# Kernel tuning notes

Hardware: AMD Instinct MI355X
Metric: run time of the kernel (lower is better)

Reference implementation:

```python
import jax, jax.numpy as jnp
import numpy as np

TAU = 1.1      # LIF membrane time constant
ALPHA = 4.0    # sigmoid surrogate sharpness (spikingjelly default)
EPS = 1e-5     # BatchNorm eps
SCALE = 0.125  # attention scale


def lif(x, v_th):
    # Single-step LIF, v init 0, decay_input=True: v = x / tau; spike = H(v - v_th)
    # Straight-through: forward heaviside, backward sigmoid surrogate derivative.
    u = x / TAU - v_th
    sg = jax.nn.sigmoid(ALPHA * u)
    return sg + jax.lax.stop_gradient((u >= 0.0).astype(x.dtype) - sg)


def bn(x, gamma, beta):
    # BatchNorm1d in training mode on [B, C, N]: stats over (B, N) per channel
    mean = jnp.mean(x, axis=(0, 2), keepdims=True)
    var = jnp.var(x, axis=(0, 2), keepdims=True)
    return gamma[None, :, None] * (x - mean) * jax.lax.rsqrt(var + EPS) + beta[None, :, None]


def conv1x1(w, x):
    # Conv1d kernel_size=1: pointwise channel mix, x: [B,C,N], w: [O,C]
    return jnp.einsum('oc,bcn->bon', w, x)


def setup_inputs() -> dict:
    key = jax.random.key(0)
    B, C, N = 32, 512, 1024
    ks = jax.random.split(key, 6)
    s = 1.0 / np.sqrt(C)
    inp = {"x": jax.random.normal(ks[0], (B, C, N), jnp.float32)}
    for name, k in zip(["q", "k", "v", "proj"], ks[1:5]):
        inp[name + "_w"] = jax.random.uniform(k, (C, C), jnp.float32, -s, s)
        inp[name + "_gamma"] = jnp.ones((C,), jnp.float32)
        inp[name + "_beta"] = jnp.zeros((C,), jnp.float32)
    inp["proj_b"] = jax.random.uniform(ks[5], (C,), jnp.float32, -s, s)
    return inp


def reference(x, q_w, q_gamma, q_beta, k_w, k_gamma, k_beta, v_w, v_gamma, v_beta,
              proj_w, proj_b, proj_gamma, proj_beta):
    # x: [B, C, N]
    q = lif(bn(conv1x1(q_w, x), q_gamma, q_beta), 1.0)  # [B,C,N] spikes
    k = lif(bn(conv1x1(k_w, x), k_gamma, k_beta), 1.0)
    v = lif(bn(conv1x1(v_w, x), v_gamma, v_beta), 1.0)
    # linear (softmax-free) attention: kv[c,d] = sum_n k[n,c] v[n,d]
    kv = jnp.einsum('bcn,bdn->bcd', k, v)               # [B,C,C]
    attn = jnp.einsum('bcn,bcd->bdn', q, kv) * SCALE    # [B,C,N] (already transposed back)
    attn = lif(attn, 0.5)
    out = conv1x1(proj_w, attn) + proj_b[None, :, None]
    return lif(bn(out, proj_gamma, proj_beta), 1.0)
```

## Files before the change

kernel.cpp:

```cpp
#include <hip/hip_runtime.h>
#include <cstddef>


#define CC 512
#define BB 32
#define NN 1024

typedef __attribute__((ext_vector_type(4))) float v4f;
typedef __attribute__((ext_vector_type(2))) float v2f;
typedef __attribute__((ext_vector_type(4))) int v4i;
typedef __attribute__((ext_vector_type(8))) int v8i;
typedef unsigned char uchar;
typedef unsigned long long ull;

__device__ __forceinline__ uchar f2e4s(float v) {
  const uchar s = (v < 0.f) ? 0x80 : 0x00;
  float a = fabsf(v);
  if (a >= 464.f) return s | 0x7E;
  if (a < 0.015625f) {
    int q = (int)rintf(a * 512.f);
    return s | (uchar)q;
  }
  const int e = (int)((__float_as_uint(a) >> 23) & 0xFF) - 126;
  const float scale = __uint_as_float((unsigned)(4 - e + 127) << 23);
  const int q = (int)rintf(a * scale);
  int code = ((e - 1 + 7) << 3) + (q - 8);
  if (code > 0x7E) code = 0x7E;
  return s | (uchar)code;
}
__device__ __forceinline__ float e42f(uchar b) {
  const int e = (b >> 3) & 15, m = b & 7;
  const float mag = e ? __uint_as_float((unsigned)((e + 120) << 23) | ((unsigned)m << 20))
                      : (float)m * 0.001953125f;
  return (b & 0x80) ? -mag : mag;
}

__device__ __forceinline__ unsigned pk4_fp8(float a0, float a1, float a2, float a3) {
#if __has_builtin(__builtin_amdgcn_cvt_pk_fp8_f32)
  int r = __builtin_amdgcn_cvt_pk_fp8_f32(a0, a1, 0, false);
  r = __builtin_amdgcn_cvt_pk_fp8_f32(a2, a3, r, true);
  return (unsigned)r;
#else
  return (unsigned)f2e4s(a0) | ((unsigned)f2e4s(a1) << 8) |
         ((unsigned)f2e4s(a2) << 16) | ((unsigned)f2e4s(a3) << 24);
#endif
}
__device__ __forceinline__ uchar enc1(float v) {
#if __has_builtin(__builtin_amdgcn_cvt_pk_fp8_f32)
  return (uchar)(__builtin_amdgcn_cvt_pk_fp8_f32(v, v, 0, false) & 0xFF);
#else
  return f2e4s(v);
#endif
}
template <bool HI>
__device__ __forceinline__ v2f dec2(int src) {
#if __has_builtin(__builtin_amdgcn_cvt_pk_f32_fp8)
  return __builtin_amdgcn_cvt_pk_f32_fp8(src, HI);
#else
  v2f r;
  const int s = HI ? (src >> 16) : src;
  r[0] = e42f((uchar)s);
  r[1] = e42f((uchar)(s >> 8));
  return r;
#endif
}
__device__ __forceinline__ float dec1(uchar b) {
#if __has_builtin(__builtin_amdgcn_cvt_f32_fp8)
  return __builtin_amdgcn_cvt_f32_fp8((int)b, 0);
#else
  return e42f(b);
#endif
}

__device__ __forceinline__ void gload16(const void* g, void* l) {
  __builtin_amdgcn_global_load_lds(
      (const __attribute__((address_space(1))) unsigned int*)g,
      (__attribute__((address_space(3))) unsigned int*)l, 16, 0, 0);
}

template <int EPI>
__global__ __launch_bounds__(256) void gemm8(const uchar* __restrict__ A,
                                             const uchar* __restrict__ B,
                                             uchar* __restrict__ Cout,
                                             const float* __restrict__ bias,
                                             int M, int N, int K,
                                             long sA, long sB, long sC) {
  __shared__ __align__(16) uchar lds[32768];
  const int b = blockIdx.z;
  const uchar* Ab = A + (size_t)b * sA;
  const uchar* Bb = B + (size_t)b * sB;
  const int m0 = blockIdx.y * 128, n0 = blockIdx.x * 128;
  const int tid = threadIdx.x;
  const int wave = tid >> 6, lane = tid & 63;
  const int lrow = lane & 15, lquad = lane >> 4;
  const int wr = wave >> 1, wc = wave & 1;

  v4f acc[4][4];
#pragma unroll
  for (int i = 0; i < 4; i++)
#pragma unroll
    for (int j = 0; j < 4; j++) acc[i][j] = (v4f)0.f;

  const uchar* gA0 = Ab + (size_t)(m0 + 32 * wave + lrow) * K + lquad * 32;
  const uchar* gA1 = gA0 + (size_t)16 * K;
  const uchar* gB0 = Bb + (size_t)(n0 + 32 * wave + lrow) * K + lquad * 32;
  const uchar* gB1 = gB0 + (size_t)16 * K;
  uchar* lA0 = lds + (2 * wave) * 2048;
  uchar* lA1 = lA0 + 2048;
  uchar* lB0 = lds + 16384 + (2 * wave) * 2048;
  uchar* lB1 = lB0 + 2048;

  for (int k0 = 0; k0 < K; k0 += 128) {
    gload16(gA0, lA0);
    gload16(gA0 + 16, lA0 + 1024);
    gload16(gA1, lA1);
    gload16(gA1 + 16, lA1 + 1024);
    gload16(gB0, lB0);
    gload16(gB0 + 16, lB0 + 1024);
    gload16(gB1, lB1);
    gload16(gB1 + 16, lB1 + 1024);
    gA0 += 128; gA1 += 128; gB0 += 128; gB1 += 128;
    __syncthreads();
    const uchar* ra = lds + (size_t)(4 * wr) * 2048 + 16 * lane;
    const uchar* rb = lds + 16384 + (size_t)(4 * wc) * 2048 + 16 * lane;
    v8i af[4], bf[4];
#pragma unroll
    for (int i = 0; i < 4; i++) {
      const v4i lo = *(const v4i*)(ra + i * 2048);
      const v4i hi = *(const v4i*)(ra + i * 2048 + 1024);
      af[i][0] = lo[0]; af[i][1] = lo[1]; af[i][2] = lo[2]; af[i][3] = lo[3];
      af[i][4] = hi[0]; af[i][5] = hi[1]; af[i][6] = hi[2]; af[i][7] = hi[3];
    }
#pragma unroll
    for (int j = 0; j < 4; j++) {
      const v4i lo = *(const v4i*)(rb + j * 2048);
      const v4i hi = *(const v4i*)(rb + j * 2048 + 1024);
      bf[j][0] = lo[0]; bf[j][1] = lo[1]; bf[j][2] = lo[2]; bf[j][3] = lo[3];
      bf[j][4] = hi[0]; bf[j][5] = hi[1]; bf[j][6] = hi[2]; bf[j][7] = hi[3];
    }
#pragma unroll
    for (int i = 0; i < 4; i++)
#pragma unroll
      for (int j = 0; j < 4; j++)
        acc[i][j] = __builtin_amdgcn_mfma_scale_f32_16x16x128_f8f6f4(
            af[i], bf[j], acc[i][j], 0, 0, 0, 127, 0, 127);
    __syncthreads();
  }

  if (EPI == 3) {
#pragma unroll
    for (int mi = 0; mi < 4; mi++)
#pragma unroll
      for (int r = 0; r < 4; r++) {
        const float bi = bias[m0 + 64 * wr + 16 * mi + lquad * 4 + r];
#pragma unroll
        for (int ni = 0; ni < 4; ni++) acc[mi][ni][r] += bi;
      }
  }

#pragma unroll
  for (int mi = 0; mi < 4; mi++) {
    const int row0 = m0 + 64 * wr + 16 * mi + lquad * 4;
#pragma unroll
    for (int ni = 0; ni < 4; ni++) {
      const int col = n0 + 64 * wc + 16 * ni + lrow;
      uchar* cp = Cout + (size_t)b * sC + (size_t)row0 * N + col;
      if (EPI == 1) {
#pragma unroll
        for (int r = 0; r < 4; r++) {
          const float u = (acc[mi][ni][r] * 0.125f) / 1.1f - 0.5f;
          cp[(size_t)r * N] = (u >= 0.f) ? (uchar)0x38 : (uchar)0;
        }
      } else {
        const unsigned pk = pk4_fp8(acc[mi][ni][0], acc[mi][ni][1],
                                    acc[mi][ni][2], acc[mi][ni][3]);
#pragma unroll
        for (int r = 0; r < 4; r++) cp[(size_t)r * N] = (uchar)(pk >> (8 * r));
      }
    }
  }
}

__global__ __launch_bounds__(256) void stats_part8_k(const uchar* __restrict__ in,
                                                     float* __restrict__ P,
                                                     long bstride) {
  const int part = blockIdx.x, c = blockIdx.y;
  const int tid = threadIdx.x;
  const int bi = part * 4 + (tid >> 6);
  const int lane = tid & 63;
  const uchar* p = in + (size_t)bi * bstride + (size_t)c * 1024 + lane * 16;
  const uint4 u = *(const uint4*)p;
  const int w4[4] = {(int)u.x, (int)u.y, (int)u.z, (int)u.w};
  float s = 0.f, s2 = 0.f;
#pragma unroll
  for (int t = 0; t < 4; t++) {
    const v2f a = dec2<false>(w4[t]);
    const v2f bb = dec2<true>(w4[t]);
    s += (a[0] + a[1]) + (bb[0] + bb[1]);
    s2 += a[0] * a[0] + a[1] * a[1] + bb[0] * bb[0] + bb[1] * bb[1];
  }
#pragma unroll
  for (int off = 32; off > 0; off >>= 1) {
    s += __shfl_down(s, off, 64);
    s2 += __shfl_down(s2, off, 64);
  }
  __shared__ float rs[4], rq[4];
  const int w = tid >> 6;
  if (lane == 0) { rs[w] = s; rq[w] = s2; }
  __syncthreads();
  if (tid == 0) {
    float2 o = make_float2(rs[0] + rs[1] + rs[2] + rs[3],
                           rq[0] + rq[1] + rq[2] + rq[3]);
    *(float2*)(P + (size_t)(c * 8 + part) * 2) = o;
  }
}

__global__ __launch_bounds__(256) void finalize8_k(const float* __restrict__ P,
                                                   float2* __restrict__ F,
                                                   const float* __restrict__ g0, const float* __restrict__ b0,
                                                   const float* __restrict__ g1, const float* __restrict__ b1,
                                                   const float* __restrict__ g2, const float* __restrict__ b2,
                                                   int nch) {
  const int c = blockIdx.x * 256 + threadIdx.x;
  if (c >= nch) return;
  const float* pc = P + (size_t)c * 16;
  float S = 0.f, Q = 0.f;
#pragma unroll
  for (int t = 0; t < 8; t++) { S += pc[2 * t]; Q += pc[2 * t + 1]; }
  const float mean = S * (1.f / 32768.f);
  const float var = fmaxf(Q * (1.f / 32768.f) - mean * mean, 0.f);
  const float rinv = 1.f / sqrtf(var + 1e-5f);
  const int sec = c >> 9, cl = c & 511;
  const float g = (sec == 0 ? g0 : sec == 1 ? g1 : g2)[cl];
  const float bt = (sec == 0 ? b0 : sec == 1 ? b1 : b2)[cl];
  const float a = g * rinv;
  F[c] = make_float2(a, bt - mean * a);
}

__global__ __launch_bounds__(256) void apply_kv8(const uchar* __restrict__ qkv8,
                                                 uchar* __restrict__ k8,
                                                 uchar* __restrict__ v8,
                                                 const float2* __restrict__ F) {
  const int sec = blockIdx.y;
  const size_t t = (size_t)blockIdx.x * 256 + threadIdx.x;
  const size_t i = t * 8;
  const int b = (int)(i >> 19);
  const int rem = (int)(i & 524287);
  const int c = rem >> 10, n = rem & 1023;
  const float2 ab = F[512 + 512 * sec + c];
  const uchar* src = qkv8 + (size_t)b * (1536 * 1024) + (size_t)(512 + 512 * sec + c) * 1024 + n;
  const uint2 u = *(const uint2*)src;
  ull packed = 0;
  {
    const v2f a = dec2<false>((int)u.x);
    const v2f bb = dec2<true>((int)u.x);
    const float f[4] = {a[0], a[1], bb[0], bb[1]};
#pragma unroll
    for (int j = 0; j < 4; j++) {
      const ull sp = (ab.x * f[j] + ab.y >= 1.1f) ? 0x38ull : 0ull;
      packed |= sp << (8 * j);
    }
  }
  {
    const v2f a = dec2<false>((int)u.y);
    const v2f bb = dec2<true>((int)u.y);
    const float f[4] = {a[0], a[1], bb[0], bb[1]};
#pragma unroll
    for (int j = 0; j < 4; j++) {
      const ull sp = (ab.x * f[j] + ab.y >= 1.1f) ? 0x38ull : 0ull;
      packed |= sp << (8 * (4 + j));
    }
  }
  uchar* dst = (sec ? v8 : k8) + (size_t)b * (CC * NN) + (size_t)c * 1024 + n;
  *(ull*)dst = packed;
}

__global__ __launch_bounds__(256) void apply_qT8(const uchar* __restrict__ qkv8,
                                                 uchar* __restrict__ q8,
                                                 const float2* __restrict__ F) {
  __shared__ uchar tile[32][33];
  const int b = blockIdx.z;
  const int n0 = blockIdx.x * 32, c0 = blockIdx.y * 32;
  const int tx = threadIdx.x & 31, ty = threadIdx.x >> 5;
  const uchar* in = qkv8 + (size_t)b * (1536 * 1024);
#pragma unroll
  for (int i = 0; i < 32; i += 8) {
    const int c = c0 + ty + i;
    const float2 ab = F[c];
    const float f = dec1(in[(size_t)c * 1024 + n0 + tx]);
    tile[ty + i][tx] = (ab.x * f + ab.y >= 1.1f) ? (uchar)0x38 : (uchar)0;
  }
  __syncthreads();
  uchar* out = q8 + (size_t)b * (NN * CC);
  const int nl = threadIdx.x >> 3;
  const int cq = (threadIdx.x & 7) * 4;
  uchar4 v;
  v.x = tile[cq][nl]; v.y = tile[cq + 1][nl];
  v.z = tile[cq + 2][nl]; v.w = tile[cq + 3][nl];
  *(uchar4*)(out + (size_t)(n0 + nl) * CC + c0 + cq) = v;
}

__global__ __launch_bounds__(256) void apply_final_k(const uchar* __restrict__ in,
                                                     float* __restrict__ outp,
                                                     const float2* __restrict__ F) {
  const size_t idx = ((size_t)blockIdx.x * 256 + threadIdx.x) * 8;
  const int c = (int)((idx >> 10) & (CC - 1));
  const float2 ab = F[c];
  const uint2 u = *(const uint2*)(in + idx);
  float of[8];
  {
    const v2f a = dec2<false>((int)u.x);
    const v2f bb = dec2<true>((int)u.x);
    of[0] = (ab.x * a[0] + ab.y >= 1.1f) ? 1.f : 0.f;
    of[1] = (ab.x * a[1] + ab.y >= 1.1f) ? 1.f : 0.f;
    of[2] = (ab.x * bb[0] + ab.y >= 1.1f) ? 1.f : 0.f;
    of[3] = (ab.x * bb[1] + ab.y >= 1.1f) ? 1.f : 0.f;
  }
  {
    const v2f a = dec2<false>((int)u.y);
    const v2f bb = dec2<true>((int)u.y);
    of[4] = (ab.x * a[0] + ab.y >= 1.1f) ? 1.f : 0.f;
    of[5] = (ab.x * a[1] + ab.y >= 1.1f) ? 1.f : 0.f;
    of[6] = (ab.x * bb[0] + ab.y >= 1.1f) ? 1.f : 0.f;
    of[7] = (ab.x * bb[1] + ab.y >= 1.1f) ? 1.f : 0.f;
  }
  float* op = outp + idx;
  *(float4*)op = make_float4(of[0], of[1], of[2], of[3]);
  *(float4*)(op + 4) = make_float4(of[4], of[5], of[6], of[7]);
}

__global__ __launch_bounds__(256) void transpose_f32_8(const float* __restrict__ inp,
                                                       uchar* __restrict__ out) {
  __shared__ uchar tile[32][33];
  const int b = blockIdx.z;
  const int n0 = blockIdx.x * 32, c0 = blockIdx.y * 32;
  const int tx = threadIdx.x & 31, ty = threadIdx.x >> 5;
  const float* in = inp + (size_t)b * (CC * NN);
#pragma unroll
  for (int i = 0; i < 32; i += 8) {
    tile[ty + i][tx] = enc1(in[(size_t)(c0 + ty + i) * NN + n0 + tx]);
  }
  __syncthreads();
  uchar* o = out + (size_t)b * (NN * CC);
  const int nl = threadIdx.x >> 3;
  const int cq = (threadIdx.x & 7) * 4;
  uchar4 v;
  v.x = tile[cq][nl]; v.y = tile[cq + 1][nl];
  v.z = tile[cq + 2][nl]; v.w = tile[cq + 3][nl];
  *(uchar4*)(o + (size_t)(n0 + nl) * CC + c0 + cq) = v;
}

__global__ __launch_bounds__(256) void wcvt8_k(const float* __restrict__ w0, const float* __restrict__ w1,
                                               const float* __restrict__ w2, const float* __restrict__ w3,
                                               uchar* __restrict__ o0, uchar* __restrict__ o1,
                                               uchar* __restrict__ o2, uchar* __restrict__ o3) {
  const float* src;
  uchar* dst;
  switch (blockIdx.y) {
    case 0: src = w0; dst = o0; break;
    case 1: src = w1; dst = o1; break;
    case 2: src = w2; dst = o2; break;
    default: src = w3; dst = o3; break;
  }
  const int i = (blockIdx.x * 256 + threadIdx.x) * 4;
  float4 v = *(const float4*)(src + i);
  *(unsigned*)(dst + i) = pk4_fp8(v.x, v.y, v.z, v.w);
}

extern "C" void kernel_launch(void* const* d_in, const int* in_sizes, int n_in,
                              void* d_out, int out_size, void* d_ws, size_t ws_size,
                              hipStream_t stream) {
  const float* x          = (const float*)d_in[0];
  const float* q_w        = (const float*)d_in[1];
  const float* q_gamma    = (const float*)d_in[2];
  const float* q_beta     = (const float*)d_in[3];
  const float* k_w        = (const float*)d_in[4];
  const float* k_gamma    = (const float*)d_in[5];
  const float* k_beta     = (const float*)d_in[6];
  const float* v_w        = (const float*)d_in[7];
  const float* v_gamma    = (const float*)d_in[8];
  const float* v_beta     = (const float*)d_in[9];
  const float* proj_w     = (const float*)d_in[10];
  const float* proj_gamma = (const float*)d_in[11];
  const float* proj_beta  = (const float*)d_in[12];
  const float* proj_b     = (const float*)d_in[13];

  char* base = (char*)d_ws;
  const size_t MB = 1u << 20;
  uchar*  xT8    = (uchar*)base;
  uchar*  qkv8   = (uchar*)(base + 16 * MB);
  uchar*  q8     = (uchar*)(base + 64 * MB);
  uchar*  k8     = (uchar*)(base + 80 * MB);
  uchar*  v8     = (uchar*)(base + 96 * MB);
  uchar*  kvT8   = (uchar*)(base + 112 * MB);
  uchar*  attnT8 = (uchar*)(base + 120 * MB);
  uchar*  outpre8= (uchar*)(base + 136 * MB);
  uchar*  wqkv8  = (uchar*)(base + 152 * MB);
  uchar*  wp8    = wqkv8 + 3 * CC * CC;
  float*  P      = (float*)(base + 154 * MB);
  float*  Pp     = P + 1536 * 16;
  float2* F      = (float2*)(Pp + 512 * 16);
  float* dout = (float*)d_out;

  const long QKVL = (long)3 * CC * NN;
  const long NCL  = (long)NN * CC;
  const long CNL  = (long)CC * NN;
  const long KVL  = (long)CC * CC;

  transpose_f32_8<<<dim3(NN / 32, CC / 32, BB), 256, 0, stream>>>(x, xT8);
  wcvt8_k<<<dim3(CC * CC / 1024, 4), 256, 0, stream>>>(
      q_w, k_w, v_w, proj_w, wqkv8, wqkv8 + CC * CC, wqkv8 + 2 * CC * CC, wp8);

  gemm8<2><<<dim3(NN / 128, 1536 / 128, BB), 256, 0, stream>>>(
      wqkv8, xT8, qkv8, nullptr, 1536, NN, CC, 0, NCL, QKVL);

  stats_part8_k<<<dim3(8, 1536), 256, 0, stream>>>(qkv8, P, QKVL);
  finalize8_k<<<6, 256, 0, stream>>>(P, F, q_gamma, q_beta, k_gamma, k_beta,
                                     v_gamma, v_beta, 1536);

  apply_qT8<<<dim3(NN / 32, CC / 32, BB), 256, 0, stream>>>(qkv8, q8, F);
  apply_kv8<<<dim3(8192, 2), 256, 0, stream>>>(qkv8, k8, v8, F);

  gemm8<0><<<dim3(CC / 128, CC / 128, BB), 256, 0, stream>>>(
      v8, k8, kvT8, nullptr, CC, CC, NN, CNL, CNL, KVL);
  gemm8<1><<<dim3(CC / 128, NN / 128, BB), 256, 0, stream>>>(
      q8, kvT8, attnT8, nullptr, NN, CC, CC, NCL, KVL, NCL);
  gemm8<3><<<dim3(NN / 128, CC / 128, BB), 256, 0, stream>>>(
      wp8, attnT8, outpre8, proj_b, CC, NN, CC, 0, NCL, CNL);

  stats_part8_k<<<dim3(8, CC), 256, 0, stream>>>(outpre8, Pp, CNL);
  finalize8_k<<<2, 256, 0, stream>>>(Pp, F, proj_gamma, proj_beta, proj_gamma,
                                     proj_beta, proj_gamma, proj_beta, CC);
  apply_final_k<<<8192, 256, 0, stream>>>(outpre8, dout, F);
}
```

Before: 326.2 us.

## Double K-step per GEMM barrier and merge prep/apply kernels into single launches

The fp8 GEMM now stages two 128-wide K slices per iteration in a 64 KB LDS buffer. This halves the number of barrier pairs per tile but doubles LDS use, which may reduce occupancy. Separately, the x transpose and weight conversion are merged into one launch, and the q-transpose and k/v spike-apply kernels into another, removing launch gaps. The q apply path also now reads four bytes per thread with packed fp8 decode instead of one byte.

After: 328.3 us. Within noise of the previous version (+0.7%).

```diff
diff --git a/kernel.cpp b/kernel.cpp
--- a/kernel.cpp
+++ b/kernel.cpp
@@ -64,13 +64,6 @@
   return r;
 #endif
 }
-__device__ __forceinline__ float dec1(uchar b) {
-#if __has_builtin(__builtin_amdgcn_cvt_f32_fp8)
-  return __builtin_amdgcn_cvt_f32_fp8((int)b, 0);
-#else
-  return e42f(b);
-#endif
-}
 
 __device__ __forceinline__ void gload16(const void* g, void* l) {
   __builtin_amdgcn_global_load_lds(
@@ -85,7 +78,7 @@
                                              const float* __restrict__ bias,
                                              int M, int N, int K,
                                              long sA, long sB, long sC) {
-  __shared__ __align__(16) uchar lds[32768];
+  __shared__ __align__(16) uchar lds[65536];
   const int b = blockIdx.z;
   const uchar* Ab = A + (size_t)b * sA;
   const uchar* Bb = B + (size_t)b * sB;
@@ -107,43 +100,51 @@
   const uchar* gB1 = gB0 + (size_t)16 * K;
   uchar* lA0 = lds + (2 * wave) * 2048;
   uchar* lA1 = lA0 + 2048;
-  uchar* lB0 = lds + 16384 + (2 * wave) * 2048;
+  uchar* lB0 = lds + 32768 + (2 * wave) * 2048;
   uchar* lB1 = lB0 + 2048;
 
-  for (int k0 = 0; k0 < K; k0 += 128) {
-    gload16(gA0, lA0);
-    gload16(gA0 + 16, lA0 + 1024);
-    gload16(gA1, lA1);
-    gload16(gA1 + 16, lA1 + 1024);
-    gload16(gB0, lB0);
-    gload16(gB0 + 16, lB0 + 1024);
-    gload16(gB1, lB1);
-    gload16(gB1 + 16, lB1 + 1024);
-    gA0 += 128; gA1 += 128; gB0 += 128; gB1 += 128;
+  for (int k0 = 0; k0 < K; k0 += 256) {
+#pragma unroll
+    for (int g = 0; g < 2; g++) {
+      const int go = g * 128;
+      const int lo = g * 16384;
+      gload16(gA0 + go,      lA0 + lo);
+      gload16(gA0 + go + 16, lA0 + lo + 1024);
+      gload16(gA1 + go,      lA1 + lo);
+      gload16(gA1 + go + 16, lA1 + lo + 1024);
+      gload16(gB0 + go,      lB0 + lo);
+      gload16(gB0 + go + 16, lB0 + lo + 1024);
+      gload16(gB1 + go,      lB1 + lo);
+      gload16(gB1 + go + 16, lB1 + lo + 1024);
+    }
+    gA0 += 256; gA1 += 256; gB0 += 256; gB1 += 256;
     __syncthreads();
-    const uchar* ra = lds + (size_t)(4 * wr) * 2048 + 16 * lane;
-    const uchar* rb = lds + 16384 + (size_t)(4 * wc) * 2048 + 16 * lane;
-    v8i af[4], bf[4];
-#pragma unroll
-    for (int i = 0; i < 4; i++) {
-      const v4i lo = *(const v4i*)(ra + i * 2048);
-      const v4i hi = *(const v4i*)(ra + i * 2048 + 1024);
-      af[i][0] = lo[0]; af[i][1] = lo[1]; af[i][2] = lo[2]; af[i][3] = lo[3];
-      af[i][4] = hi[0]; af[i][5] = hi[1]; af[i][6] = hi[2]; af[i][7] = hi[3];
-    }
-#pragma unroll
-    for (int j = 0; j < 4; j++) {
-      const v4i lo = *(const v4i*)(rb + j * 2048);
-      const v4i hi = *(const v4i*)(rb + j * 2048 + 1024);
-      bf[j][0] = lo[0]; bf[j][1] = lo[1]; bf[j][2] = lo[2]; bf[j][3] = lo[3];
-      bf[j][4] = hi[0]; bf[j][5] = hi[1]; bf[j][6] = hi[2]; bf[j][7] = hi[3];
-    }
-#pragma unroll
-    for (int i = 0; i < 4; i++)
-#pragma unroll
-      for (int j = 0; j < 4; j++)
-        acc[i][j] = __builtin_amdgcn_mfma_scale_f32_16x16x128_f8f6f4(
-            af[i], bf[j], acc[i][j], 0, 0, 0, 127, 0, 127);
+#pragma unroll
+    for (int g = 0; g < 2; g++) {
+      const uchar* ra = lds + g * 16384 + (size_t)(4 * wr) * 2048 + 16 * lane;
+      const uchar* rb = lds + 32768 + g * 16384 + (size_t)(4 * wc) * 2048 + 16 * lane;
+      v8i af[4], bf[4];
+#pragma unroll
+      for (int i = 0; i < 4; i++) {
+        const v4i lo4 = *(const v4i*)(ra + i * 2048);
+        const v4i hi4 = *(const v4i*)(ra + i * 2048 + 1024);
+        af[i][0] = lo4[0]; af[i][1] = lo4[1]; af[i][2] = lo4[2]; af[i][3] = lo4[3];
+        af[i][4] = hi4[0]; af[i][5] = hi4[1]; af[i][6] = hi4[2]; af[i][7] = hi4[3];
+      }
+#pragma unroll
+      for (int j = 0; j < 4; j++) {
+        const v4i lo4 = *(const v4i*)(rb + j * 2048);
+        const v4i hi4 = *(const v4i*)(rb + j * 2048 + 1024);
+        bf[j][0] = lo4[0]; bf[j][1] = lo4[1]; bf[j][2] = lo4[2]; bf[j][3] = lo4[3];
+        bf[j][4] = hi4[0]; bf[j][5] = hi4[1]; bf[j][6] = hi4[2]; bf[j][7] = hi4[3];
+      }
+#pragma unroll
+      for (int i = 0; i < 4; i++)
+#pragma unroll
+        for (int j = 0; j < 4; j++)
+          acc[i][j] = __builtin_amdgcn_mfma_scale_f32_16x16x128_f8f6f4(
+              af[i], bf[j], acc[i][j], 0, 0, 0, 127, 0, 127);
+    }
     __syncthreads();
   }
 
@@ -237,67 +238,68 @@
   F[c] = make_float2(a, bt - mean * a);
 }
 
-__global__ __launch_bounds__(256) void apply_kv8(const uchar* __restrict__ qkv8,
-                                                 uchar* __restrict__ k8,
-                                                 uchar* __restrict__ v8,
-                                                 const float2* __restrict__ F) {
-  const int sec = blockIdx.y;
-  const size_t t = (size_t)blockIdx.x * 256 + threadIdx.x;
-  const size_t i = t * 8;
-  const int b = (int)(i >> 19);
-  const int rem = (int)(i & 524287);
-  const int c = rem >> 10, n = rem & 1023;
-  const float2 ab = F[512 + 512 * sec + c];
-  const uchar* src = qkv8 + (size_t)b * (1536 * 1024) + (size_t)(512 + 512 * sec + c) * 1024 + n;
-  const uint2 u = *(const uint2*)src;
-  ull packed = 0;
-  {
-    const v2f a = dec2<false>((int)u.x);
-    const v2f bb = dec2<true>((int)u.x);
-    const float f[4] = {a[0], a[1], bb[0], bb[1]};
-#pragma unroll
-    for (int j = 0; j < 4; j++) {
-      const ull sp = (ab.x * f[j] + ab.y >= 1.1f) ? 0x38ull : 0ull;
-      packed |= sp << (8 * j);
-    }
-  }
-  {
-    const v2f a = dec2<false>((int)u.y);
-    const v2f bb = dec2<true>((int)u.y);
-    const float f[4] = {a[0], a[1], bb[0], bb[1]};
-#pragma unroll
-    for (int j = 0; j < 4; j++) {
-      const ull sp = (ab.x * f[j] + ab.y >= 1.1f) ? 0x38ull : 0ull;
-      packed |= sp << (8 * (4 + j));
-    }
-  }
-  uchar* dst = (sec ? v8 : k8) + (size_t)b * (CC * NN) + (size_t)c * 1024 + n;
-  *(ull*)dst = packed;
-}
-
-__global__ __launch_bounds__(256) void apply_qT8(const uchar* __restrict__ qkv8,
-                                                 uchar* __restrict__ q8,
-                                                 const float2* __restrict__ F) {
-  __shared__ uchar tile[32][33];
-  const int b = blockIdx.z;
-  const int n0 = blockIdx.x * 32, c0 = blockIdx.y * 32;
-  const int tx = threadIdx.x & 31, ty = threadIdx.x >> 5;
-  const uchar* in = qkv8 + (size_t)b * (1536 * 1024);
-#pragma unroll
-  for (int i = 0; i < 32; i += 8) {
-    const int c = c0 + ty + i;
-    const float2 ab = F[c];
-    const float f = dec1(in[(size_t)c * 1024 + n0 + tx]);
-    tile[ty + i][tx] = (ab.x * f + ab.y >= 1.1f) ? (uchar)0x38 : (uchar)0;
-  }
-  __syncthreads();
-  uchar* out = q8 + (size_t)b * (NN * CC);
-  const int nl = threadIdx.x >> 3;
-  const int cq = (threadIdx.x & 7) * 4;
-  uchar4 v;
-  v.x = tile[cq][nl]; v.y = tile[cq + 1][nl];
-  v.z = tile[cq + 2][nl]; v.w = tile[cq + 3][nl];
-  *(uchar4*)(out + (size_t)(n0 + nl) * CC + c0 + cq) = v;
+__global__ __launch_bounds__(256) void apply_all_k(const uchar* __restrict__ qkv8,
+                                                   uchar* __restrict__ q8,
+                                                   uchar* __restrict__ k8,
+                                                   uchar* __restrict__ v8,
+                                                   const float2* __restrict__ F) {
+  const int bid = blockIdx.x;
+  const int tid = threadIdx.x;
+  if (bid < 16384) {
+    __shared__ uchar tile[32][33];
+    const int nb = bid & 31, cb = (bid >> 5) & 15, b = bid >> 9;
+    const int n0 = nb * 32, c0 = cb * 32;
+    const uchar* in = qkv8 + (size_t)b * (1536 * 1024);
+    const int cl = tid >> 3;
+    const int n4 = (tid & 7) * 4;
+    const float2 ab = F[c0 + cl];
+    const unsigned w = *(const unsigned*)(in + (size_t)(c0 + cl) * 1024 + n0 + n4);
+    const v2f a = dec2<false>((int)w);
+    const v2f bb = dec2<true>((int)w);
+    tile[cl][n4 + 0] = (ab.x * a[0] + ab.y >= 1.1f) ? (uchar)0x38 : (uchar)0;
+    tile[cl][n4 + 1] = (ab.x * a[1] + ab.y >= 1.1f) ? (uchar)0x38 : (uchar)0;
+    tile[cl][n4 + 2] = (ab.x * bb[0] + ab.y >= 1.1f) ? (uchar)0x38 : (uchar)0;
+    tile[cl][n4 + 3] = (ab.x * bb[1] + ab.y >= 1.1f) ? (uchar)0x38 : (uchar)0;
+    __syncthreads();
+    uchar* out = q8 + (size_t)b * (NN * CC);
+    const int nl = tid >> 3;
+    const int cq = (tid & 7) * 4;
+    uchar4 v;
+    v.x = tile[cq][nl]; v.y = tile[cq + 1][nl];
+    v.z = tile[cq + 2][nl]; v.w = tile[cq + 3][nl];
+    *(uchar4*)(out + (size_t)(n0 + nl) * CC + c0 + cq) = v;
+  } else {
+    const int t0 = bid - 16384;
+    const int sec = t0 >> 13;
+    const int blk = t0 & 8191;
+    const size_t t = (size_t)blk * 256 + tid;
+    const size_t i = t * 8;
+    const int b = (int)(i >> 19);
+    const int rem = (int)(i & 524287);
+    const int c = rem >> 10, n = rem & 1023;
+    const float2 ab = F[512 + 512 * sec + c];
+    const uchar* src = qkv8 + (size_t)b * (1536 * 1024) + (size_t)(512 + 512 * sec + c) * 1024 + n;
+    const uint2 u = *(const uint2*)src;
+    ull packed = 0;
+    {
+      const v2f a = dec2<false>((int)u.x);
+      const v2f bb = dec2<true>((int)u.x);
+      const float f[4] = {a[0], a[1], bb[0], bb[1]};
+#pragma unroll
+      for (int j = 0; j < 4; j++)
+        packed |= ((ab.x * f[j] + ab.y >= 1.1f) ? 0x38ull : 0ull) << (8 * j);
+    }
+    {
+      const v2f a = dec2<false>((int)u.y);
+      const v2f bb = dec2<true>((int)u.y);
+      const float f[4] = {a[0], a[1], bb[0], bb[1]};
+#pragma unroll
+      for (int j = 0; j < 4; j++)
+        packed |= ((ab.x * f[j] + ab.y >= 1.1f) ? 0x38ull : 0ull) << (8 * (4 + j));
+    }
+    uchar* dst = (sec ? v8 : k8) + (size_t)b * (CC * NN) + (size_t)c * 1024 + n;
+    *(ull*)dst = packed;
+  }
 }
 
 __global__ __launch_bounds__(256) void apply_final_k(const uchar* __restrict__ in,
@@ -329,42 +331,41 @@
   *(float4*)(op + 4) = make_float4(of[4], of[5], of[6], of[7]);
 }
 
-__global__ __launch_bounds__(256) void transpose_f32_8(const float* __restrict__ inp,
-                                                       uchar* __restrict__ out) {
-  __shared__ uchar tile[32][33];
-  const int b = blockIdx.z;
-  const int n0 = blockIdx.x * 32, c0 = blockIdx.y * 32;
-  const int tx = threadIdx.x & 31, ty = threadIdx.x >> 5;
-  const float* in = inp + (size_t)b * (CC * NN);
-#pragma unroll
-  for (int i = 0; i < 32; i += 8) {
-    tile[ty + i][tx] = enc1(in[(size_t)(c0 + ty + i) * NN + n0 + tx]);
-  }
-  __syncthreads();
-  uchar* o = out + (size_t)b * (NN * CC);
-  const int nl = threadIdx.x >> 3;
-  const int cq = (threadIdx.x & 7) * 4;
-  uchar4 v;
-  v.x = tile[cq][nl]; v.y = tile[cq + 1][nl];
-  v.z = tile[cq + 2][nl]; v.w = tile[cq + 3][nl];
-  *(uchar4*)(o + (size_t)(n0 + nl) * CC + c0 + cq) = v;
-}
-
-__global__ __launch_bounds__(256) void wcvt8_k(const float* __restrict__ w0, const float* __restrict__ w1,
-                                               const float* __restrict__ w2, const float* __restrict__ w3,
-                                               uchar* __restrict__ o0, uchar* __restrict__ o1,
-                                               uchar* __restrict__ o2, uchar* __restrict__ o3) {
-  const float* src;
-  uchar* dst;
-  switch (blockIdx.y) {
-    case 0: src = w0; dst = o0; break;
-    case 1: src = w1; dst = o1; break;
-    case 2: src = w2; dst = o2; break;
-    default: src = w3; dst = o3; break;
-  }
-  const int i = (blockIdx.x * 256 + threadIdx.x) * 4;
-  float4 v = *(const float4*)(src + i);
-  *(unsigned*)(dst + i) = pk4_fp8(v.x, v.y, v.z, v.w);
+__global__ __launch_bounds__(256) void prep_k(const float* __restrict__ x,
+                                              const float* __restrict__ w0, const float* __restrict__ w1,
+                                              const float* __restrict__ w2, const float* __restrict__ w3,
+                                              uchar* __restrict__ xT8,
+                                              uchar* __restrict__ o0, uchar* __restrict__ o1,
+                                              uchar* __restrict__ o2, uchar* __restrict__ o3) {
+  const int bid = blockIdx.x;
+  const int tid = threadIdx.x;
+  if (bid < 16384) {
+    __shared__ uchar tile[32][33];
+    const int nb = bid & 31, cb = (bid >> 5) & 15, b = bid >> 9;
+    const int n0 = nb * 32, c0 = cb * 32;
+    const float* in = x + (size_t)b * (CC * NN);
+    const int tx = tid & 31, ty = tid >> 5;
+#pragma unroll
+    for (int i = 0; i < 32; i += 8) {
+      tile[ty + i][tx] = enc1(in[(size_t)(c0 + ty + i) * NN + n0 + tx]);
+    }
+    __syncthreads();
+    uchar* o = xT8 + (size_t)b * (NN * CC);
+    const int nl = tid >> 3;
+    const int cq = (tid & 7) * 4;
+    uchar4 v;
+    v.x = tile[cq][nl]; v.y = tile[cq + 1][nl];
+    v.z = tile[cq + 2][nl]; v.w = tile[cq + 3][nl];
+    *(uchar4*)(o + (size_t)(n0 + nl) * CC + c0 + cq) = v;
+  } else {
+    const int t = bid - 16384;
+    const int mat = t >> 8, blk = t & 255;
+    const float* src = (mat == 0) ? w0 : (mat == 1) ? w1 : (mat == 2) ? w2 : w3;
+    uchar* dst = (mat == 0) ? o0 : (mat == 1) ? o1 : (mat == 2) ? o2 : o3;
+    const int i = (blk * 256 + tid) * 4;
+    float4 v = *(const float4*)(src + i);
+    *(unsigned*)(dst + i) = pk4_fp8(v.x, v.y, v.z, v.w);
+  }
 }
 
 extern "C" void kernel_launch(void* const* d_in, const int* in_sizes, int n_in,
@@ -407,9 +408,8 @@
   const long CNL  = (long)CC * NN;
   const long KVL  = (long)CC * CC;
 
-  transpose_f32_8<<<dim3(NN / 32, CC / 32, BB), 256, 0, stream>>>(x, xT8);
-  wcvt8_k<<<dim3(CC * CC / 1024, 4), 256, 0, stream>>>(
-      q_w, k_w, v_w, proj_w, wqkv8, wqkv8 + CC * CC, wqkv8 + 2 * CC * CC, wp8);
+  prep_k<<<17408, 256, 0, stream>>>(x, q_w, k_w, v_w, proj_w, xT8,
+                                    wqkv8, wqkv8 + CC * CC, wqkv8 + 2 * CC * CC, wp8);
 
   gemm8<2><<<dim3(NN / 128, 1536 / 128, BB), 256, 0, stream>>>(
       wqkv8, xT8, qkv8, nullptr, 1536, NN, CC, 0, NCL, QKVL);
@@ -418,8 +418,7 @@
   finalize8_k<<<6, 256, 0, stream>>>(P, F, q_gamma, q_beta, k_gamma, k_beta,
                                      v_gamma, v_beta, 1536);
 
-  apply_qT8<<<dim3(NN / 32, CC / 32, BB), 256, 0, stream>>>(qkv8, q8, F);
-  apply_kv8<<<dim3(8192, 2), 256, 0, stream>>>(qkv8, k8, v8, F);
+  apply_all_k<<<32768, 256, 0, stream>>>(qkv8, q8, k8, v8, F);
 
   gemm8<0><<<dim3(CC / 128, CC / 128, BB), 256, 0, stream>>>(
       v8, k8, kvT8, nullptr, CC, CC, NN, CNL, CNL, KVL);
```
